# Performance work log

Measured on AMD Instinct MI355X. Metric: run time of the kernel, lower is better.

## Reference

```python
import jax, jax.numpy as jnp
import numpy as np

B, N, D = 4, 1024, 1024
H, KV, HD = 16, 4, 64
S, CTX = 128, 2048
MLPD = 4096
NITER, DT = 2, 0.1


def _rms(x, w, eps=1e-6):
    return x * jax.lax.rsqrt(jnp.mean(x * x, axis=-1, keepdims=True) + eps) * w


def _gelu(x):
    return jax.nn.gelu(x, approximate=False)  # torch nn.GELU() is exact erf


def _rope(q, k, cos, sin):
    # q: [B,H,N,HD], cos/sin: [N, HD//2]; interleaved-half RoPE as in source
    q1, q2 = q[..., ::2], q[..., 1::2]
    k1, k2 = k[..., ::2], k[..., 1::2]
    c = cos[None, None]
    s = sin[None, None]
    q_rot = jnp.concatenate([q1 * c - q2 * s, q1 * s + q2 * c], axis=-1)
    k_rot = jnp.concatenate([k1 * c - k2 * s, k1 * s + k2 * c], axis=-1)
    return q_rot, k_rot


def setup_inputs():
    key = jax.random.key(0)
    ks = jax.random.split(key, 24)
    rn = lambda k, shp, s=0.02: jax.random.normal(k, shp, jnp.float32) * s
    inv = 1.0 / (10000.0 ** (jnp.arange(0, HD, 2, dtype=jnp.float32) / HD))  # [HD//2]
    ang = jnp.arange(N, dtype=jnp.float32)[:, None] * inv[None, :]
    return {
        'x': jax.random.normal(ks[0], (B, N, D), jnp.float32),
        'c': jax.random.normal(ks[1], (B, D), jnp.float32),
        'context': jax.random.normal(ks[2], (B, S, CTX), jnp.float32),
        'cos': jnp.cos(ang), 'sin': jnp.sin(ang),
        'wq': rn(ks[3], (D, D)), 'wk': rn(ks[4], (D, KV * HD)),
        'wv': rn(ks[5], (D, KV * HD)), 'wo': rn(ks[6], (D, D)),
        'cwq': rn(ks[7], (D, D)), 'cwk': rn(ks[8], (CTX, D)),
        'cwv': rn(ks[9], (CTX, D)), 'cwo': rn(ks[10], (D, D)),
        'fc1_w': rn(ks[11], (D, MLPD)), 'fc1_b': jnp.zeros((MLPD,), jnp.float32),
        'fc2_w': rn(ks[12], (MLPD, D)), 'fc2_b': jnp.zeros((D,), jnp.float32),
        'ada_w': rn(ks[13], (D, 6 * D)), 'ada_b': jnp.zeros((6 * D,), jnp.float32),
        'n1': jnp.ones((D,), jnp.float32), 'n2': jnp.ones((D,), jnp.float32), 'n3': jnp.ones((D,), jnp.float32),
        'int_w': jnp.full((D,), 0.5, jnp.float32), 'mu': jnp.zeros((D,), jnp.float32),
        'hg1_w': rn(ks[14], (D, D // 4)), 'hg1_b': jnp.zeros((D // 4,), jnp.float32),
        'hg2_w': rn(ks[15], (D // 4, 1)), 'hg2_b': jnp.zeros((1,), jnp.float32),
        'ct1_w': rn(ks[16], (2 * D, D // 2)), 'ct1_b': jnp.zeros((D // 2,), jnp.float32),
        'ct2_w': rn(ks[17], (D // 2, 3 * D)), 'ct2_b': jnp.zeros((3 * D,), jnp.float32),
        'rf1_w': rn(ks[18], (D, 2 * D)), 'rf1_b': jnp.zeros((2 * D,), jnp.float32),
        'rf2_w': rn(ks[19], (2 * D, D)), 'rf2_b': jnp.zeros((D,), jnp.float32),
    }


def _forward(x, c, context, cos, sin, wq, wk, wv, wo, cwq, cwk, cwv, cwo,
             fc1_w, fc1_b, fc2_w, fc2_b, ada_w, ada_b, n1, n2, n3, int_w, mu,
             hg1_w, hg1_b, hg2_w, hg2_b, ct1_w, ct1_b, ct2_w, ct2_b,
             rf1_w, rf1_b, rf2_w, rf2_b):
    scale = HD ** -0.5
    # AdaLN-Zero modulation from timestep conditioning c: [B, 6D]
    mod = jax.nn.silu(c) @ ada_w + ada_b
    sh_msa, sc_msa, g_msa, sh_mlp, sc_mlp, g_mlp = jnp.split(mod, 6, axis=-1)
    # --- GQA self-attention with RoPE ---
    h = _rms(x, n1) * (1.0 + sc_msa[:, None, :]) + sh_msa[:, None, :]
    q = (h @ wq).reshape(B, N, H, HD).transpose(0, 2, 1, 3)
    k = (h @ wk).reshape(B, N, KV, HD).transpose(0, 2, 1, 3)
    v = (h @ wv).reshape(B, N, KV, HD).transpose(0, 2, 1, 3)
    q, k = _rope(q, k, cos, sin)
    k = jnp.repeat(k, H // KV, axis=1)  # repeat_interleave over head dim
    v = jnp.repeat(v, H // KV, axis=1)
    attn = jax.nn.softmax(jnp.einsum('bhnd,bhmd->bhnm', q, k) * scale, axis=-1)
    sa = jnp.einsum('bhnm,bhmd->bhnd', attn, v).transpose(0, 2, 1, 3).reshape(B, N, D) @ wo
    x = x + g_msa[:, None, :] * sa
    # --- cross-attention (text conditioning) ---
    h2 = _rms(x, n2)
    qc = (h2 @ cwq).reshape(B, N, H, HD).transpose(0, 2, 1, 3)
    kc = (context @ cwk).reshape(B, S, H, HD).transpose(0, 2, 1, 3)
    vc = (context @ cwv).reshape(B, S, H, HD).transpose(0, 2, 1, 3)
    ca = jax.nn.softmax(jnp.einsum('bhnd,bhsd->bhns', qc, kc) * scale, axis=-1)
    xa = jnp.einsum('bhns,bhsd->bhnd', ca, vc).transpose(0, 2, 1, 3).reshape(B, N, D) @ cwo
    x = x + xa
    # --- AdaLN-modulated MLP ---
    h3 = _rms(x, n3) * (1.0 + sc_mlp[:, None, :]) + sh_mlp[:, None, :]
    m = _gelu(h3 @ fc1_w + fc1_b) @ fc2_w + fc2_b
    x = x + g_mlp[:, None, :] * m
    # --- IntegratorNeuron: damped-oscillator halting dynamics ---
    vst = jnp.zeros_like(x)
    integ = x
    halt_probs = []
    for _ in range(NITER):
        ctrl = _gelu(jnp.concatenate([integ, vst], axis=-1) @ ct1_w + ct1_b) @ ct2_w + ct2_b
        a_raw, b_raw, g_raw = jnp.split(ctrl, 3, axis=-1)
        alpha = jax.nn.sigmoid(a_raw)
        beta = jax.nn.softplus(b_raw)
        gate = jax.nn.sigmoid(g_raw)
        v_next = alpha * vst - beta * (integ - mu)
        x_next = integ + DT * gate * v_next
        hp = jax.nn.sigmoid(_gelu(x_next @ hg1_w + hg1_b) @ hg2_w + hg2_b)  # [B,N,1]
        refined = _gelu(x_next @ rf1_w + rf1_b) @ rf2_w + rf2_b
        integ = integ + hp * refined * int_w
        vst = v_next
        halt_probs.append(hp)
    return integ, jnp.stack(halt_probs, axis=1)


def reference(x, c, context, cos, sin, wq, wk, wv, wo, cwq, cwk, cwv, cwo,
              fc1_w, fc1_b, fc2_w, fc2_b, ada_w, ada_b, n1, n2, n3, int_w, mu,
              hg1_w, hg1_b, hg2_w, hg2_b, ct1_w, ct1_b, ct2_w, ct2_b,
              rf1_w, rf1_b, rf2_w, rf2_b):
    return _forward(x, c, context, cos, sin, wq, wk, wv, wo, cwq, cwk, cwv, cwo,
                    fc1_w, fc1_b, fc2_w, fc2_b, ada_w, ada_b, n1, n2, n3, int_w, mu,
                    hg1_w, hg1_b, hg2_w, hg2_b, ct1_w, ct1_b, ct2_w, ct2_b,
                    rf1_w, rf1_b, rf2_w, rf2_b)
```

## Files before the change

### kernel.cpp

```cpp
#include <hip/hip_runtime.h>
#include <hip/hip_bf16.h>
#include <math.h>

typedef __hip_bfloat16 bf16;
typedef unsigned short ushort;
typedef __bf16 bf16x8 __attribute__((ext_vector_type(8)));
typedef unsigned short u16x8 __attribute__((ext_vector_type(8)));
typedef float f32x4 __attribute__((ext_vector_type(4)));

#define BB 4
#define NN 1024
#define DD 1024
#define HH 16
#define KVH 4
#define HDIM 64
#define SS 128
#define CTXD 2048
#define MLPDIM 4096

__device__ __forceinline__ float bf2f(bf16 v){ return __bfloat162float(v); }
__device__ __forceinline__ bf16 f2bf(float v){ return __float2bfloat16(v); }
__device__ __forceinline__ ushort fbits(float v){ bf16 h = __float2bfloat16(v); return *(ushort*)&h; }
__device__ __forceinline__ float ubf(ushort u){ unsigned int x = ((unsigned int)u) << 16; float f; *(unsigned int*)&f = x; return f; }
__device__ __forceinline__ float sigmf_(float x){ return 1.f/(1.f+expf(-x)); }
__device__ __forceinline__ float geluf_(float x){ return 0.5f*x*(1.f+erff(x*0.70710678118f)); }

typedef const __attribute__((address_space(1))) void* gas_t;
typedef __attribute__((address_space(3))) void* las_t;
__device__ __forceinline__ void gl2lds16(const void* g, void* l){
  __builtin_amdgcn_global_load_lds((gas_t)g, (las_t)l, 16, 0, 0);
}

__global__ void k_copy4(const float4* __restrict__ in, float4* __restrict__ out, int n4){
  int i = blockIdx.x*256 + threadIdx.x;
  if (i < n4) out[i] = in[i];
}
__global__ void k_f2bfv(const float* __restrict__ in, bf16* __restrict__ out, int n){
  int i = blockIdx.x*256 + threadIdx.x;
  if (i < n) out[i] = f2bf(in[i]);
}
__global__ void k_silu(const float* __restrict__ c, float* __restrict__ out, int n){
  int i = blockIdx.x*256 + threadIdx.x;
  if (i < n){ float v = c[i]; out[i] = v*sigmf_(v); }
}
__global__ void k_zero16(unsigned short* __restrict__ p, int n){
  int i = blockIdx.x*256 + threadIdx.x;
  if (i < n) p[i] = 0;
}

__global__ __launch_bounds__(256) void k_wt(const float* __restrict__ in, bf16* __restrict__ out, int K, int N){
  __shared__ float t[64][65];
  int bn = blockIdx.x*64, bk = blockIdx.y*64;
  int tid = threadIdx.x;
  int c4 = (tid & 15)*4, r = tid >> 4;
  #pragma unroll
  for (int i = 0; i < 4; ++i){
    float4 v = *(const float4*)(in + (size_t)(bk + r + i*16)*N + bn + c4);
    t[c4+0][r+i*16] = v.x; t[c4+1][r+i*16] = v.y; t[c4+2][r+i*16] = v.z; t[c4+3][r+i*16] = v.w;
  }
  __syncthreads();
  int n = tid >> 2, k16 = (tid & 3)*16;
  bf16* orow = out + (size_t)(bn + n)*K + bk + k16;
  #pragma unroll
  for (int j = 0; j < 16; ++j) orow[j] = f2bf(t[n][k16 + j]);
}

__global__ void k_ada(const float* __restrict__ sc, const float* __restrict__ w,
                      const float* __restrict__ b, float* __restrict__ mod){
  int idx = blockIdx.x*256 + threadIdx.x;
  int bb = idx / 6144, col = idx % 6144;
  const float* cp = sc + bb*DD;
  float s = 0.f;
  for (int k = 0; k < DD; ++k) s += cp[k]*w[(size_t)k*6144 + col];
  mod[idx] = s + b[col];
}

__global__ __launch_bounds__(256) void k_rms(const float* __restrict__ X, const float* __restrict__ w,
                      const float* __restrict__ mod, int sc_off, int sh_off,
                      bf16* __restrict__ out, int use_mod){
  __shared__ float red[256];
  int row = blockIdx.x;
  int b = row >> 10;
  int tid = threadIdx.x;
  const float* xr = X + (size_t)row*DD;
  float s = 0.f;
  #pragma unroll
  for (int i = 0; i < 4; ++i){ float v = xr[tid + i*256]; s += v*v; }
  red[tid] = s; __syncthreads();
  for (int st = 128; st > 0; st >>= 1){ if (tid < st) red[tid] += red[tid+st]; __syncthreads(); }
  float rstd = rsqrtf(red[0]*(1.f/DD) + 1e-6f);
  bf16* orow = out + (size_t)row*DD;
  const float* mrow = use_mod ? (mod + (size_t)b*6*DD) : nullptr;
  #pragma unroll
  for (int i = 0; i < 4; ++i){
    int d = tid + i*256;
    float v = xr[d]*rstd*w[d];
    if (use_mod) v = v*(1.f + mrow[sc_off + d]) + mrow[sh_off + d];
    orow[d] = f2bf(v);
  }
}

__global__ __launch_bounds__(256,2) void k_mm2(const ushort* __restrict__ A, const ushort* __restrict__ BT,
                      const float* __restrict__ bias, ushort* __restrict__ C,
                      int M, int N, int K, int act){
  __shared__ ushort As[128*64];
  __shared__ ushort Bs[128*64];
  int tid = threadIdx.x, lane = tid & 63, wv = tid >> 6;
  int l15 = lane & 15, quad = lane >> 4;
  int bm = blockIdx.y*128, bn = blockIdx.x*128;
  int wm = (wv & 1)*64, wn = (wv >> 1)*64;
  int lr = lane >> 3, lc = lane & 7;
  int ksw = (lc ^ lr) << 3;
  f32x4 acc[4][4] = {};
  const ushort* Abase = A  + (size_t)(bm + wv*32 + lr)*K + ksw;
  const ushort* Bbase = BT + (size_t)(bn + wv*32 + lr)*K + ksw;
  ushort* AsW = As + wv*2048;
  ushort* BsW = Bs + wv*2048;
  int swr = (l15 & 7) << 3;
  for (int k0 = 0; k0 < K; k0 += 64){
    #pragma unroll
    for (int i = 0; i < 4; ++i){
      gl2lds16(Abase + k0 + (size_t)(i*8)*K, AsW + i*512);
      gl2lds16(Bbase + k0 + (size_t)(i*8)*K, BsW + i*512);
    }
    __syncthreads();
    #pragma unroll
    for (int ks = 0; ks < 2; ++ks){
      bf16x8 af[4], bfr[4];
      #pragma unroll
      for (int mi = 0; mi < 4; ++mi){
        int r = wm + mi*16 + l15;
        af[mi] = __builtin_bit_cast(bf16x8, *(const uint4*)(As + r*64 + ((ks*32 + quad*8) ^ swr)));
      }
      #pragma unroll
      for (int nj = 0; nj < 4; ++nj){
        int r = wn + nj*16 + l15;
        bfr[nj] = __builtin_bit_cast(bf16x8, *(const uint4*)(Bs + r*64 + ((ks*32 + quad*8) ^ swr)));
      }
      #pragma unroll
      for (int mi = 0; mi < 4; ++mi)
        #pragma unroll
        for (int nj = 0; nj < 4; ++nj)
          acc[mi][nj] = __builtin_amdgcn_mfma_f32_16x16x32_bf16(af[mi], bfr[nj], acc[mi][nj], 0, 0, 0);
    }
    __syncthreads();
  }
  #pragma unroll
  for (int nj = 0; nj < 4; ++nj){
    int col = bn + wn + nj*16 + l15;
    float bv = bias ? bias[col] : 0.f;
    #pragma unroll
    for (int mi = 0; mi < 4; ++mi){
      #pragma unroll
      for (int r = 0; r < 4; ++r){
        int row = bm + wm + mi*16 + quad*4 + r;
        float v = acc[mi][nj][r] + bv;
        if (act) v = geluf_(v);
        C[(size_t)row*N + col] = fbits(v);
      }
    }
  }
}

__global__ void k_rope(const bf16* __restrict__ in, const float* __restrict__ cw,
                       const float* __restrict__ sw, bf16* __restrict__ out, int NHp, int n){
  int idx = blockIdx.x*256 + threadIdx.x;
  if (idx >= n) return;
  int d2 = idx & 31; int t = idx >> 5;
  int nn = t % NN; t /= NN; int h = t % NHp; int b = t / NHp;
  const bf16* base = in + ((size_t)((b*NN+nn)*NHp + h))*HDIM;
  float e = bf2f(base[2*d2]), o = bf2f(base[2*d2+1]);
  float c = cw[nn*32 + d2], s = sw[nn*32 + d2];
  bf16* ob = out + ((size_t)((b*NHp+h)*NN + nn))*HDIM;
  ob[d2]      = f2bf(e*c - o*s);
  ob[32 + d2] = f2bf(e*s + o*c);
}

__global__ void k_tr(const bf16* __restrict__ in, bf16* __restrict__ out, int T, int NHp, int n){
  int idx = blockIdx.x*256 + threadIdx.x;
  if (idx >= n) return;
  int d = idx & 63; int t = idx >> 6;
  int h = t % NHp; t /= NHp; int tok = t % T; int b = t / T;
  out[((size_t)((b*NHp+h)*T + tok))*64 + d] = in[idx];
}

__global__ void k_trv(const bf16* __restrict__ in, bf16* __restrict__ out, int T, int NHp, int n){
  int idx = blockIdx.x*256 + threadIdx.x;
  if (idx >= n) return;
  int d = idx & 63; int t = idx >> 6;
  int h = t % NHp; t /= NHp; int tok = t % T; int b = t / T;
  out[((size_t)(b*NHp+h)*64 + d)*T + tok] = in[idx];
}

__global__ __launch_bounds__(256) void k_fattn(const ushort* __restrict__ Q, const ushort* __restrict__ K,
                      const ushort* __restrict__ V, ushort* __restrict__ O,
                      int NH, int NKV, int Nq, int Nk, float scale){
  __shared__ ushort Kt[64*72];
  __shared__ ushort Vt[64*72];
  __shared__ ushort Ps[4][16*72];
  int tid = threadIdx.x, lane = tid & 63, wv = tid >> 6;
  int l15 = lane & 15, quad = lane >> 4;
  int nqt = Nq >> 6;
  int qt = blockIdx.x % nqt; int t = blockIdx.x / nqt; int h = t % NH; int b = t / NH;
  int kvh = h / (NH / NKV);
  const ushort* Kb = K + (size_t)(b*NKV+kvh)*Nk*64;
  const ushort* Vb = V + (size_t)(b*NKV+kvh)*64*Nk;
  const ushort* Qp = Q + ((size_t)((b*NH+h)*Nq + qt*64 + wv*16 + l15))*64;
  bf16x8 qf0 = __builtin_bit_cast(bf16x8, *(const uint4*)(Qp + quad*8));
  bf16x8 qf1 = __builtin_bit_cast(bf16x8, *(const uint4*)(Qp + 32 + quad*8));
  f32x4 acc[4] = {};
  float m_run[4] = {-1e30f,-1e30f,-1e30f,-1e30f};
  float l_run[4] = {0.f,0.f,0.f,0.f};
  ushort* Pw = Ps[wv];
  for (int t0 = 0; t0 < Nk; t0 += 64){
    #pragma unroll
    for (int i = 0; i < 2; ++i){
      int c = tid + i*256; int row = c >> 3; int k8 = (c & 7) << 3;
      *(uint4*)(Kt + row*72 + k8) = *(const uint4*)(Kb + (size_t)(t0+row)*64 + k8);
      *(uint4*)(Vt + row*72 + k8) = *(const uint4*)(Vb + (size_t)row*Nk + t0 + k8);
    }
    __syncthreads();
    f32x4 s[4] = {};
    #pragma unroll
    for (int nj = 0; nj < 4; ++nj){
      bf16x8 kf0 = __builtin_bit_cast(bf16x8, *(const uint4*)(Kt + (nj*16+l15)*72 + quad*8));
      s[nj] = __builtin_amdgcn_mfma_f32_16x16x32_bf16(qf0, kf0, s[nj], 0, 0, 0);
      bf16x8 kf1 = __builtin_bit_cast(bf16x8, *(const uint4*)(Kt + (nj*16+l15)*72 + 32 + quad*8));
      s[nj] = __builtin_amdgcn_mfma_f32_16x16x32_bf16(qf1, kf1, s[nj], 0, 0, 0);
    }
    #pragma unroll
    for (int nj = 0; nj < 4; ++nj)
      #pragma unroll
      for (int r = 0; r < 4; ++r) s[nj][r] *= scale;
    float al[4];
    #pragma unroll
    for (int r = 0; r < 4; ++r){
      float tm = fmaxf(fmaxf(s[0][r], s[1][r]), fmaxf(s[2][r], s[3][r]));
      #pragma unroll
      for (int off = 8; off; off >>= 1) tm = fmaxf(tm, __shfl_xor(tm, off, 64));
      float mn = fmaxf(m_run[r], tm);
      al[r] = expf(m_run[r] - mn);
      m_run[r] = mn;
      float ts = 0.f;
      #pragma unroll
      for (int nj = 0; nj < 4; ++nj){ float p = expf(s[nj][r] - mn); s[nj][r] = p; ts += p; }
      #pragma unroll
      for (int off = 8; off; off >>= 1) ts += __shfl_xor(ts, off, 64);
      l_run[r] = l_run[r]*al[r] + ts;
    }
    #pragma unroll
    for (int nj = 0; nj < 4; ++nj){
      #pragma unroll
      for (int r = 0; r < 4; ++r){
        acc[nj][r] *= al[r];
        Pw[(quad*4+r)*72 + nj*16 + l15] = fbits(s[nj][r]);
      }
    }
    bf16x8 pf0 = __builtin_bit_cast(bf16x8, *(const uint4*)(Pw + l15*72 + quad*8));
    bf16x8 pf1 = __builtin_bit_cast(bf16x8, *(const uint4*)(Pw + l15*72 + 32 + quad*8));
    #pragma unroll
    for (int nj = 0; nj < 4; ++nj){
      bf16x8 vf0 = __builtin_bit_cast(bf16x8, *(const uint4*)(Vt + (nj*16+l15)*72 + quad*8));
      acc[nj] = __builtin_amdgcn_mfma_f32_16x16x32_bf16(pf0, vf0, acc[nj], 0, 0, 0);
      bf16x8 vf1 = __builtin_bit_cast(bf16x8, *(const uint4*)(Vt + (nj*16+l15)*72 + 32 + quad*8));
      acc[nj] = __builtin_amdgcn_mfma_f32_16x16x32_bf16(pf1, vf1, acc[nj], 0, 0, 0);
    }
    __syncthreads();
  }
  float inv[4];
  #pragma unroll
  for (int r = 0; r < 4; ++r) inv[r] = 1.f / l_run[r];
  int nbase = qt*64 + wv*16 + quad*4;
  #pragma unroll
  for (int r = 0; r < 4; ++r){
    size_t ob = ((size_t)((b*Nq + nbase + r)*NH + h))*64;
    #pragma unroll
    for (int nj = 0; nj < 4; ++nj)
      O[ob + nj*16 + l15] = fbits(acc[nj][r]*inv[r]);
  }
}

__global__ void k_resid(float* __restrict__ X, const bf16* __restrict__ val,
                        const float* __restrict__ mod, int goff, int n){
  int i = blockIdx.x*256 + threadIdx.x;
  if (i >= n) return;
  float g = 1.f;
  if (mod){ int b = i >> 20; int d = i & 1023; g = mod[b*6144 + goff + d]; }
  X[i] += g*bf2f(val[i]);
}

__global__ void k_concat(const float* __restrict__ X, const bf16* __restrict__ V,
                         bf16* __restrict__ C, int n){
  int i = blockIdx.x*256 + threadIdx.x;
  if (i >= n) return;
  int row = i >> 11, col = i & 2047;
  C[i] = (col < 1024) ? f2bf(X[(size_t)row*1024 + col]) : V[(size_t)row*1024 + col - 1024];
}

__global__ void k_ctrl(const bf16* __restrict__ ctrl, const float* __restrict__ X,
                       bf16* __restrict__ VST, bf16* __restrict__ XN,
                       const float* __restrict__ mu, int n){
  int i = blockIdx.x*256 + threadIdx.x;
  if (i >= n) return;
  int row = i >> 10, d = i & 1023;
  const bf16* cr = ctrl + (size_t)row*3072;
  float alpha = sigmf_(bf2f(cr[d]));
  float braw  = bf2f(cr[1024 + d]);
  float beta  = fmaxf(braw, 0.f) + log1pf(expf(-fabsf(braw)));
  float gate  = sigmf_(bf2f(cr[2048 + d]));
  float vn = alpha*bf2f(VST[i]) - beta*(X[i] - mu[d]);
  VST[i] = f2bf(vn);
  XN[i]  = f2bf(X[i] + 0.1f*gate*vn);
}

__global__ __launch_bounds__(64) void k_hg2(const bf16* __restrict__ hin, const float* __restrict__ w,
                     const float* __restrict__ bb, float* __restrict__ hp,
                     float* __restrict__ oout, int it){
  int r = blockIdx.x; int lane = threadIdx.x;
  const bf16* hr = hin + (size_t)r*256;
  float s = 0.f;
  #pragma unroll
  for (int i = 0; i < 4; ++i) s += bf2f(hr[lane + i*64])*w[lane + i*64];
  for (int off = 32; off; off >>= 1) s += __shfl_xor(s, off, 64);
  if (lane == 0){
    float v = sigmf_(s + bb[0]);
    hp[r] = v;
    int b = r >> 10, nn = r & 1023;
    oout[((size_t)(b*2 + it) << 10) + nn] = v;
  }
}

__global__ void k_integ(float* __restrict__ X, const float* __restrict__ hp,
                        const bf16* __restrict__ rf, const float* __restrict__ iw, int n){
  int i = blockIdx.x*256 + threadIdx.x;
  if (i >= n) return;
  int row = i >> 10, d = i & 1023;
  X[i] += hp[row]*bf2f(rf[i])*iw[d];
}

extern "C" void kernel_launch(void* const* d_in, const int* in_sizes, int n_in,
                              void* d_out, int out_size, void* d_ws, size_t ws_size,
                              hipStream_t stream) {
  const float* x_in  = (const float*)d_in[0];
  const float* c_in  = (const float*)d_in[1];
  const float* ctx_in= (const float*)d_in[2];
  const float* cosw  = (const float*)d_in[3];
  const float* sinw  = (const float*)d_in[4];
  const float* wq    = (const float*)d_in[5];
  const float* wk    = (const float*)d_in[6];
  const float* wv    = (const float*)d_in[7];
  const float* wo    = (const float*)d_in[8];
  const float* cwq   = (const float*)d_in[9];
  const float* cwk   = (const float*)d_in[10];
  const float* cwv   = (const float*)d_in[11];
  const float* cwo   = (const float*)d_in[12];
  const float* fc1_w = (const float*)d_in[13];
  const float* fc1_b = (const float*)d_in[14];
  const float* fc2_w = (const float*)d_in[15];
  const float* fc2_b = (const float*)d_in[16];
  const float* ada_w = (const float*)d_in[17];
  const float* ada_b = (const float*)d_in[18];
  const float* n1    = (const float*)d_in[19];
  const float* n2    = (const float*)d_in[20];
  const float* n3    = (const float*)d_in[21];
  const float* int_w = (const float*)d_in[22];
  const float* mu    = (const float*)d_in[23];
  const float* hg1_w = (const float*)d_in[24];
  const float* hg1_b = (const float*)d_in[25];
  const float* hg2_w = (const float*)d_in[26];
  const float* hg2_b = (const float*)d_in[27];
  const float* ct1_w = (const float*)d_in[28];
  const float* ct1_b = (const float*)d_in[29];
  const float* ct2_w = (const float*)d_in[30];
  const float* ct2_b = (const float*)d_in[31];
  const float* rf1_w = (const float*)d_in[32];
  const float* rf1_b = (const float*)d_in[33];
  const float* rf2_w = (const float*)d_in[34];
  const float* rf2_b = (const float*)d_in[35];

  float* out_f  = (float*)d_out;
  float* out_hp = out_f + (size_t)BB*NN*DD;

  char* wsb = (char*)d_ws;
  const size_t Mi = 1u << 20;
  float* X  = (float*)wsb;
  bf16*  Hh = (bf16*)(wsb + 16*Mi);
  bf16*  Qb = (bf16*)(wsb + 24*Mi);
  bf16*  R  = (bf16*)(wsb + 32*Mi);
  bf16*  QR  = R;
  bf16*  SAb = R + 4*Mi;
  bf16*  KP  = R + 8*Mi;
  bf16*  VP  = R + 9*Mi;
  bf16*  KR  = R + 10*Mi;
  bf16*  VR  = R + 11*Mi;
  bf16*  CTXB= R + 12*Mi;
  bf16*  BIG = R;
  bf16*  CT1 = R + 12*Mi;
  bf16*  HG1 = R + 12*Mi;
  bf16*  RFO = R + 8*Mi;
  float* SIL = (float*)(wsb + 64*Mi);
  float* MOD = SIL + 4096;
  float* HP  = MOD + 24576;
  bf16*  VST = Qb;
  bf16*  XN  = Hh;
  bf16* WT   = (bf16*)(wsb + 65*Mi);
  bf16* wqT  = WT;
  bf16* wkT  = wqT  + 1048576;
  bf16* wvT  = wkT  + 262144;
  bf16* woT  = wvT  + 262144;
  bf16* cwqT = woT  + 1048576;
  bf16* cwkT = cwqT + 1048576;
  bf16* cwvT = cwkT + 2097152;
  bf16* cwoT = cwvT + 2097152;
  bf16* fc1T = cwoT + 1048576;
  bf16* fc2T = fc1T + 4194304;
  bf16* ct1T = fc2T + 4194304;
  bf16* ct2T = ct1T + 1048576;
  bf16* rf1T = ct2T + 1572864;
  bf16* rf2T = rf1T + 2097152;
  bf16* hg1T = rf2T + 2097152;

  const int NT = BB*NN*DD;
  const float scale = 0.125f;
  #define G1(n) dim3(((n)+255)/256), dim3(256)
  #define WTR(src,dst,K,N) k_wt<<<dim3((N)/64,(K)/64), dim3(256), 0, stream>>>((src),(dst),(K),(N))
  #define MM(Aptr,BTptr,biasptr,Cptr,M,N,K,act) \
    k_mm2<<<dim3((N)/128,(M)/128), dim3(256), 0, stream>>>((const ushort*)(Aptr),(const ushort*)(BTptr),(biasptr),(ushort*)(Cptr),(M),(N),(K),(act))

  WTR(wq,   wqT, 1024, 1024);
  WTR(wk,   wkT, 1024, 256);
  WTR(wv,   wvT, 1024, 256);
  WTR(wo,   woT, 1024, 1024);
  WTR(cwq,  cwqT,1024, 1024);
  WTR(cwk,  cwkT,2048, 1024);
  WTR(cwv,  cwvT,2048, 1024);
  WTR(cwo,  cwoT,1024, 1024);
  WTR(fc1_w,fc1T,1024, 4096);
  WTR(fc2_w,fc2T,4096, 1024);
  WTR(ct1_w,ct1T,2048, 512);
  WTR(ct2_w,ct2T,512,  3072);
  WTR(rf1_w,rf1T,1024, 2048);
  WTR(rf2_w,rf2T,2048, 1024);
  WTR(hg1_w,hg1T,1024, 256);

  k_copy4<<<G1(NT/4), 0, stream>>>((const float4*)x_in, (float4*)X, NT/4);
  k_silu<<<G1(BB*DD), 0, stream>>>(c_in, SIL, BB*DD);
  k_ada<<<dim3(96), dim3(256), 0, stream>>>(SIL, ada_w, ada_b, MOD);

  k_rms<<<dim3(4096), dim3(256), 0, stream>>>(X, n1, MOD, DD, 0, Hh, 1);
  MM(Hh, wqT, nullptr, Qb, 4096, 1024, 1024, 0);
  MM(Hh, wkT, nullptr, KP, 4096, 256, 1024, 0);
  MM(Hh, wvT, nullptr, VP, 4096, 256, 1024, 0);
  k_rope<<<G1(BB*HH*NN*32), 0, stream>>>(Qb, cosw, sinw, QR, HH, BB*HH*NN*32);
  k_rope<<<G1(BB*KVH*NN*32), 0, stream>>>(KP, cosw, sinw, KR, KVH, BB*KVH*NN*32);
  k_trv<<<G1(BB*NN*KVH*64), 0, stream>>>(VP, VR, NN, KVH, BB*NN*KVH*64);
  k_fattn<<<dim3(BB*HH*(NN/64)), dim3(256), 0, stream>>>((const ushort*)QR, (const ushort*)KR,
      (const ushort*)VR, (ushort*)SAb, HH, KVH, NN, NN, scale);
  MM(SAb, woT, nullptr, Hh, 4096, 1024, 1024, 0);
  k_resid<<<G1(NT), 0, stream>>>(X, Hh, MOD, 2*DD, NT);

  k_rms<<<dim3(4096), dim3(256), 0, stream>>>(X, n2, nullptr, 0, 0, Hh, 0);
  MM(Hh, cwqT, nullptr, Qb, 4096, 1024, 1024, 0);
  k_tr<<<G1(NT), 0, stream>>>(Qb, QR, NN, HH, NT);
  k_f2bfv<<<G1(BB*SS*CTXD), 0, stream>>>(ctx_in, CTXB, BB*SS*CTXD);
  MM(CTXB, cwkT, nullptr, KP, 512, 1024, 2048, 0);
  MM(CTXB, cwvT, nullptr, VP, 512, 1024, 2048, 0);
  k_tr<<<G1(BB*SS*HH*64), 0, stream>>>(KP, KR, SS, HH, BB*SS*HH*64);
  k_trv<<<G1(BB*SS*HH*64), 0, stream>>>(VP, VR, SS, HH, BB*SS*HH*64);
  k_fattn<<<dim3(BB*HH*(NN/64)), dim3(256), 0, stream>>>((const ushort*)QR, (const ushort*)KR,
      (const ushort*)VR, (ushort*)SAb, HH, HH, NN, SS, scale);
  MM(SAb, cwoT, nullptr, Hh, 4096, 1024, 1024, 0);
  k_resid<<<G1(NT), 0, stream>>>(X, Hh, nullptr, 0, NT);

  k_rms<<<dim3(4096), dim3(256), 0, stream>>>(X, n3, MOD, 4*DD, 3*DD, Hh, 1);
  MM(Hh, fc1T, fc1_b, BIG, 4096, 4096, 1024, 1);
  MM(BIG, fc2T, fc2_b, Qb, 4096, 1024, 4096, 0);
  k_resid<<<G1(NT), 0, stream>>>(X, Qb, MOD, 5*DD, NT);

  k_zero16<<<G1(NT), 0, stream>>>((unsigned short*)VST, NT);
  for (int it = 0; it < 2; ++it){
    k_concat<<<G1(2*NT), 0, stream>>>(X, VST, BIG, 2*NT);
    MM(BIG, ct1T, ct1_b, CT1, 4096, 512, 2048, 1);
    MM(CT1, ct2T, ct2_b, BIG, 4096, 3072, 512, 0);
    k_ctrl<<<G1(NT), 0, stream>>>(BIG, X, VST, XN, mu, NT);
    MM(XN, hg1T, hg1_b, HG1, 4096, 256, 1024, 1);
    k_hg2<<<dim3(4096), dim3(64), 0, stream>>>(HG1, hg2_w, hg2_b, HP, out_hp, it);
    MM(XN, rf1T, rf1_b, BIG, 4096, 2048, 1024, 1);
    MM(BIG, rf2T, rf2_b, RFO, 4096, 1024, 2048, 0);
    k_integ<<<G1(NT), 0, stream>>>(X, HP, RFO, int_w, NT);
  }
  k_copy4<<<G1(NT/4), 0, stream>>>((const float4*)X, (float4*)out_f, NT/4);
  #undef G1
  #undef WTR
  #undef MM
}
```

Baseline: 1.285 ms.

## Split-K parallelize adaLN modulation GEMV with batch reuse and atomic accumulation

Replaces the serial per-output adaLN projection, which looped over the full K dimension in only 96 blocks and re-read the weight matrix once per batch row, with a split-K kernel. Each block handles 32 K rows and 1024 columns using float4 loads, reusing each weight element across all 4 batch rows. Partial sums are accumulated with atomicAdd into a buffer pre-initialized with the bias by a separate kernel. This adds one launch and atomic contention, and makes the summation order nondeterministic.

```diff
diff --git a/kernel.cpp b/kernel.cpp
--- a/kernel.cpp
+++ b/kernel.cpp
@@ -65,14 +65,32 @@
   for (int j = 0; j < 16; ++j) orow[j] = f2bf(t[n][k16 + j]);
 }
 
-__global__ void k_ada(const float* __restrict__ sc, const float* __restrict__ w,
-                      const float* __restrict__ b, float* __restrict__ mod){
+__global__ void k_adab(const float* __restrict__ b, float* __restrict__ mod, int n){
   int idx = blockIdx.x*256 + threadIdx.x;
-  int bb = idx / 6144, col = idx % 6144;
-  const float* cp = sc + bb*DD;
-  float s = 0.f;
-  for (int k = 0; k < DD; ++k) s += cp[k]*w[(size_t)k*6144 + col];
-  mod[idx] = s + b[col];
+  if (idx < n) mod[idx] = b[idx % 6144];
+}
+__global__ __launch_bounds__(256) void k_ada2(const float* __restrict__ sc, const float* __restrict__ w,
+                       float* __restrict__ mod){
+  __shared__ float sl[4][32];
+  int tid = threadIdx.x;
+  int col4 = blockIdx.x*1024 + tid*4;
+  int k0 = blockIdx.y*32;
+  if (tid < 128) sl[tid >> 5][tid & 31] = sc[(tid >> 5)*DD + k0 + (tid & 31)];
+  __syncthreads();
+  f32x4 acc[4] = {};
+  for (int kk = 0; kk < 32; ++kk){
+    const float4 wv4 = *(const float4*)(w + (size_t)(k0 + kk)*6144 + col4);
+    #pragma unroll
+    for (int b = 0; b < 4; ++b){
+      float s = sl[b][kk];
+      acc[b][0] += s*wv4.x; acc[b][1] += s*wv4.y; acc[b][2] += s*wv4.z; acc[b][3] += s*wv4.w;
+    }
+  }
+  #pragma unroll
+  for (int b = 0; b < 4; ++b)
+    #pragma unroll
+    for (int j = 0; j < 4; ++j)
+      atomicAdd(&mod[(size_t)b*6144 + col4 + j], acc[b][j]);
 }
 
 __global__ __launch_bounds__(256) void k_rms(const float* __restrict__ X, const float* __restrict__ w,
@@ -445,7 +463,8 @@
 
   k_copy4<<<G1(NT/4), 0, stream>>>((const float4*)x_in, (float4*)X, NT/4);
   k_silu<<<G1(BB*DD), 0, stream>>>(c_in, SIL, BB*DD);
-  k_ada<<<dim3(96), dim3(256), 0, stream>>>(SIL, ada_w, ada_b, MOD);
+  k_adab<<<G1(BB*6144), 0, stream>>>(ada_b, MOD, BB*6144);
+  k_ada2<<<dim3(6,32), dim3(256), 0, stream>>>(SIL, ada_w, MOD);
 
   k_rms<<<dim3(4096), dim3(256), 0, stream>>>(X, n1, MOD, DD, 0, Hh, 1);
   MM(Hh, wqT, nullptr, Qb, 4096, 1024, 1024, 0);
```

After: 1.172 ms. 1.1x faster.
